# Performance work log

Measured on AMD Instinct MI355X. Metric: run time of the kernel, lower is better.

## Reference

```python
import jax, jax.numpy as jnp
import numpy as np

BN_EPS = 1e-5
K, D = 512, 64  # vocab_size, embed_dim


def conv2d(x, w, b, stride):
    y = jax.lax.conv_general_dilated(
        x, w, window_strides=(stride, stride), padding=[(1, 1), (1, 1)],
        dimension_numbers=("NCHW", "OIHW", "NCHW"))
    return y + b[None, :, None, None]


def batchnorm(x, g, b):
    # training-mode BN: batch statistics over (N, H, W)
    m = jnp.mean(x, axis=(0, 2, 3), keepdims=True)
    v = jnp.var(x, axis=(0, 2, 3), keepdims=True)
    return (x - m) * jax.lax.rsqrt(v + BN_EPS) * g[None, :, None, None] + b[None, :, None, None]


def setup_inputs() -> dict:
    key = jax.random.key(0)
    ks = jax.random.split(key, 8)
    dims = [3, 64, 128, 256]
    inp = {"x": jax.random.normal(ks[0], (32, 3, 256, 256), dtype=jnp.float32)}
    for i in range(3):
        cin, cout = dims[i], dims[i + 1]
        inp[f"w{i+1}"] = jax.random.normal(ks[i + 1], (cout, cin, 4, 4), dtype=jnp.float32) * 0.05
        inp[f"b{i+1}"] = jnp.zeros((cout,), dtype=jnp.float32)
        inp[f"g{i+1}"] = jnp.ones((cout,), dtype=jnp.float32)
        inp[f"be{i+1}"] = jnp.zeros((cout,), dtype=jnp.float32)
    inp["wq"] = jax.random.normal(ks[4], (D, 256, 1, 1), dtype=jnp.float32) * 0.05
    inp["bq"] = jnp.zeros((D,), dtype=jnp.float32)
    inp["codebook"] = jax.random.uniform(ks[5], (K, D), dtype=jnp.float32,
                                         minval=-1.0 / K, maxval=1.0 / K)
    return inp


def reference(x, w1, b1, g1, be1, w2, b2, g2, be2, w3, b3, g3, be3, wq, bq, codebook):
    commitment_cost = 0.25
    h = jax.nn.relu(batchnorm(conv2d(x, w1, b1, 2), g1, be1))
    h = jax.nn.relu(batchnorm(conv2d(h, w2, b2, 2), g2, be2))
    h = jax.nn.relu(batchnorm(conv2d(h, w3, b3, 2), g3, be3))
    z = conv2d(h, wq, bq, 1)                      # (B, D, H', W')

    zt = jnp.transpose(z, (0, 2, 3, 1))           # (B, H', W', D)
    z_flat = zt.reshape(-1, D)                    # (N, D)
    # squared L2 distances via expansion
    dists = (jnp.sum(z_flat ** 2, axis=1, keepdims=True)
             + jnp.sum(codebook ** 2, axis=1)
             - 2.0 * z_flat @ codebook.T)         # (N, K)
    idx = jnp.argmin(dists, axis=1)               # (N,)
    quantized = codebook[idx].reshape(zt.shape)   # gather == one-hot matmul

    e_latent = jnp.mean((jax.lax.stop_gradient(quantized) - zt) ** 2)
    q_latent = jnp.mean((quantized - jax.lax.stop_gradient(zt)) ** 2)
    loss = q_latent + commitment_cost * e_latent

    # straight-through estimator
    quantized = zt + jax.lax.stop_gradient(quantized - zt)

    counts = jnp.zeros((K,), dtype=jnp.float32).at[idx].add(1.0)
    avg_probs = counts / z_flat.shape[0]
    perplexity = jnp.exp(-jnp.sum(avg_probs * jnp.log(avg_probs + 1e-10)))

    symbols = jnp.transpose(quantized, (0, 3, 1, 2))  # (B, D, H', W')
    return symbols, loss, perplexity
```

## Files before the change

kernel.cpp:

```cpp
#include <hip/hip_runtime.h>
#include <hip/hip_bf16.h>


#define BATCH 32

#define SYM_N 2367488
#define NPX   36992.0
#define CHW   73984
#define HW2   1156

static const unsigned long long NEED1 = 201392128ull;
static const unsigned long long NEED2 = 100728832ull;

typedef _Float16 half4 __attribute__((ext_vector_type(4)));
typedef _Float16 half8 __attribute__((ext_vector_type(8)));
typedef float f32x16 __attribute__((ext_vector_type(16)));

__device__ __forceinline__ float ldv(const float* p) { return *p; }
__device__ __forceinline__ float ldv(const __hip_bfloat16* p) { return __bfloat162float(*p); }
__device__ __forceinline__ float ldv(const _Float16* p) { return (float)(*p); }
__device__ __forceinline__ void stv(float* p, float v) { *p = v; }
__device__ __forceinline__ void stv(__hip_bfloat16* p, float v) { *p = __float2bfloat16(v); }
__device__ __forceinline__ void stv(_Float16* p, float v) { *p = (_Float16)v; }

__device__ __forceinline__ void st4(float* p, float a, float b, float c, float d) {
    float4 v; v.x = a; v.y = b; v.z = c; v.w = d;
    *(float4*)p = v;
}
__device__ __forceinline__ void st4(_Float16* p, float a, float b, float c, float d) {
    union { _Float16 h[4]; ushort4 u; } t;
    t.h[0] = (_Float16)a; t.h[1] = (_Float16)b; t.h[2] = (_Float16)c; t.h[3] = (_Float16)d;
    *(ushort4*)p = t.u;
}

__global__ void initStatsK(double* statd, int* counts) {
    int i = threadIdx.x + blockIdx.x * blockDim.x;
    if (i < 1537) statd[i] = 0.0;
    if (i < 512) counts[i] = 0;
}

__global__ void csqK(const float* __restrict__ cb, float* __restrict__ csqf,
                     double* __restrict__ csqd) {
    int k = threadIdx.x + blockIdx.x * blockDim.x;
    if (k < 512) {
        const float* r = cb + (size_t)k * 64;
        float s = 0.f; double sd = 0.0;
        for (int d = 0; d < 64; ++d) {
            s = fmaf(r[d], r[d], s);
            sd += (double)r[d] * (double)r[d];
        }
        csqf[k] = s; csqd[k] = sd;
    }
}

__global__ void borderK(const double* __restrict__ csqd, int* __restrict__ kborder,
                        int* __restrict__ counts, double* __restrict__ lossAcc) {
    __shared__ double sV[512];
    __shared__ int sI[512];
    const int t = threadIdx.x;
    sV[t] = csqd[t]; sI[t] = t;
    __syncthreads();
    for (int st = 256; st > 0; st >>= 1) {
        if (t < st) {
            double v2 = sV[t + st]; int i2 = sI[t + st];
            if (v2 < sV[t] || (v2 == sV[t] && i2 < sI[t])) { sV[t] = v2; sI[t] = i2; }
        }
        __syncthreads();
    }
    if (t == 0) {
        int k = sI[0];
        *kborder = k;
        atomicAdd(&counts[k], 4224);
        atomicAdd(lossAcc, 4224.0 * sV[0]);
    }
}

__global__ __launch_bounds__(256) void fillK(const int* __restrict__ kborder,
                                             const float* __restrict__ cb,
                                             float* __restrict__ out) {
    const int kb = *kborder;
    int E = blockIdx.x * 256 + threadIdx.x;
    if (E < SYM_N) {
        int d = (E / HW2) & 63;
        out[E] = cb[(size_t)kb * 64 + d];
    }
}

template<int CIN, int COUT, int IH, int IW, bool BN_IN, bool STORE, bool STATS,
         typename TI, typename TO>
__global__ __launch_bounds__(256) void conv4x4s2K(
    const TI* __restrict__ in, const float* __restrict__ wgt,
    const float* __restrict__ bias,
    const float* __restrict__ inScale, const float* __restrict__ inShift,
    TO* __restrict__ out, double* __restrict__ gSum, double* __restrict__ gSq)
{
    constexpr int OH = IH / 2, OW = IW / 2;
    constexpr int COLB = OW / 16;
    __shared__ float sIn[8 * 18 * 34];
    __shared__ float sW[128 * 64];
    __shared__ float sStat[128];

    const int tid = threadIdx.x;
    const int tx = tid & 15, ty = tid >> 4;
    const int cog = ty & 7, rg = ty >> 3;
    const int n = blockIdx.z;
    const int coBase = blockIdx.y * 64;
    const int brow = blockIdx.x / COLB, bcol = blockIdx.x % COLB;
    const int oh0 = brow * 8, ow0 = bcol * 16;
    const int ihb = oh0 * 2 - 1, iwb = ow0 * 2 - 1;

    float acc[8][4];
#pragma unroll
    for (int j = 0; j < 8; ++j)
#pragma unroll
        for (int r = 0; r < 4; ++r) acc[j][r] = 0.f;

    for (int c0 = 0; c0 < CIN; c0 += 8) {
        const int CC = (CIN - c0 < 8) ? (CIN - c0) : 8;
        for (int i = tid; i < 8 * 18 * 34; i += 256) {
            int ci = i / 612; int rem = i - ci * 612;
            int ih = rem / 34; int iw = rem - ih * 34;
            float v = 0.f;
            int gh = ihb + ih, gw = iwb + iw;
            if (ci < CC && (unsigned)gh < (unsigned)IH && (unsigned)gw < (unsigned)IW) {
                float r0 = ldv(&in[(((size_t)n * CIN + (c0 + ci)) * IH + gh) * IW + gw]);
                if (BN_IN) r0 = fmaxf(fmaf(r0, inScale[c0 + ci], inShift[c0 + ci]), 0.f);
                v = r0;
            }
            sIn[i] = v;
        }
        for (int i = tid; i < 8192; i += 256) {
            int co = i >> 7, r = i & 127;
            int ci = r >> 4, t = r & 15;
            float v = 0.f;
            if (ci < CC) v = wgt[(((size_t)(coBase + co)) * CIN + (c0 + ci)) * 16 + t];
            sW[r * 64 + (co ^ ((r & 7) << 3))] = v;
        }
        __syncthreads();
        for (int ci = 0; ci < CC; ++ci) {
#pragma unroll
            for (int kh = 0; kh < 4; ++kh) {
#pragma unroll
                for (int kw = 0; kw < 4; ++kw) {
                    const int tap = kh * 4 + kw;
                    const float* wp = sW + (ci * 16 + tap) * 64 + ((cog * 8) ^ ((tap & 7) << 3));
                    float4 wa = *(const float4*)wp;
                    float4 wb = *(const float4*)(wp + 4);
                    const float* ip = sIn + (ci * 18 + rg * 8 + kh) * 34 + tx * 2 + kw;
                    float wv[8] = {wa.x, wa.y, wa.z, wa.w, wb.x, wb.y, wb.z, wb.w};
                    float iv[4] = {ip[0], ip[68], ip[136], ip[204]};
#pragma unroll
                    for (int j = 0; j < 8; ++j)
#pragma unroll
                        for (int r = 0; r < 4; ++r)
                            acc[j][r] = fmaf(wv[j], iv[r], acc[j][r]);
                }
            }
        }
        __syncthreads();
    }

    if (STATS) {
        if (tid < 128) sStat[tid] = 0.f;
        __syncthreads();
    }

    const int coG = coBase + cog * 8;
#pragma unroll
    for (int j = 0; j < 8; ++j) {
        float bv = bias[coG + j];
        float s = 0.f, s2 = 0.f;
#pragma unroll
        for (int r = 0; r < 4; ++r) {
            float v = acc[j][r] + bv;
            if (STORE)
                stv(&out[(((size_t)n * COUT + coG + j) * OH + (oh0 + rg * 4 + r)) * OW + ow0 + tx], v);
            s += v; s2 = fmaf(v, v, s2);
        }
        if (STATS) {
#pragma unroll
            for (int m = 1; m < 16; m <<= 1) {
                s  += __shfl_xor(s, m, 64);
                s2 += __shfl_xor(s2, m, 64);
            }
            if (tx == 0) {
                atomicAdd(&sStat[cog * 8 + j], s);
                atomicAdd(&sStat[64 + cog * 8 + j], s2);
            }
        }
    }
    if (STATS) {
        __syncthreads();
        if (tid < 64) {
            atomicAdd(&gSum[coBase + tid], (double)sStat[tid]);
            atomicAdd(&gSq[coBase + tid],  (double)sStat[64 + tid]);
        }
    }
}

template<int CIN, int COUT, int IH, int IW, int TH, int TW, bool BN_IN,
         bool STORE, bool STATS, typename TI, typename TO>
__global__ __launch_bounds__(256, 3) void conv8K(
    const TI* __restrict__ in, const float* __restrict__ wgt,
    const float* __restrict__ bias,
    const float* __restrict__ inScale, const float* __restrict__ inShift,
    TO* __restrict__ out, double* __restrict__ gSum, double* __restrict__ gSq)
{
    constexpr int OH = IH / 2, OW = IW / 2;
    constexpr int COLB = OW / TW;
    constexpr int SW = TW / 2;
    constexpr int ITH = TH * 2 + 2;
    constexpr int ITWP = TW * 2 + 4;
    constexpr int INSZ = 4 * ITH * ITWP;

    __shared__ float sIn[INSZ];
    __shared__ float sW[4 * 16 * 64];
    __shared__ float sStat[128];

    const int tid = threadIdx.x;
    const int s = tid & 31, cog = tid >> 5;
    const int sw = s & (SW - 1), sh = s / SW;
    const int n = blockIdx.z;
    const int coBase = blockIdx.y * 64;
    const int brow = blockIdx.x / COLB, bcol = blockIdx.x % COLB;
    const int oh0 = brow * TH, ow0 = bcol * TW;
    const int ihb = oh0 * 2 - 1, iwb = ow0 * 2 - 1;

    float acc[8][8];
#pragma unroll
    for (int c = 0; c < 8; ++c)
#pragma unroll
        for (int p = 0; p < 8; ++p) acc[c][p] = 0.f;

    for (int c0 = 0; c0 < CIN; c0 += 4) {
        const int CC = (CIN - c0 < 4) ? (CIN - c0) : 4;
        for (int i = tid; i < INSZ; i += 256) {
            int ci = i / (ITH * ITWP); int rem = i - ci * (ITH * ITWP);
            int ih = rem / ITWP; int iw = rem - ih * ITWP;
            float v = 0.f;
            int gh = ihb + ih, gw = iwb + iw;
            if (ci < CC && (unsigned)gh < (unsigned)IH && (unsigned)gw < (unsigned)IW) {
                float r0 = ldv(&in[(((size_t)n * CIN + (c0 + ci)) * IH + gh) * IW + gw]);
                if (BN_IN) r0 = fmaxf(fmaf(r0, inScale[c0 + ci], inShift[c0 + ci]), 0.f);
                v = r0;
            }
            sIn[i] = v;
        }
        for (int i = tid; i < 4096; i += 256) {
            int r = i >> 6, co = i & 63;
            int ci = r >> 4, tap = r & 15;
            float v = (ci < CC) ? wgt[(((size_t)(coBase + co)) * CIN + (c0 + ci)) * 16 + tap] : 0.f;
            sW[r * 64 + co] = v;
        }
        __syncthreads();
        for (int ci = 0; ci < CC; ++ci) {
#pragma unroll
            for (int kh = 0; kh < 4; ++kh) {
                float inv[4][8];
#pragma unroll
                for (int r = 0; r < 4; ++r) {
                    const float* ip = sIn + (ci * ITH + (sh * 4 + r) * 2 + kh) * ITWP + sw * 4;
                    float4 a = *(const float4*)ip;
                    float4 b = *(const float4*)(ip + 4);
                    inv[r][0] = a.x; inv[r][1] = a.y; inv[r][2] = a.z; inv[r][3] = a.w;
                    inv[r][4] = b.x; inv[r][5] = b.y; inv[r][6] = b.z; inv[r][7] = b.w;
                }
#pragma unroll
                for (int kw = 0; kw < 4; ++kw) {
                    const float* wp = sW + (ci * 16 + kh * 4 + kw) * 64 + cog * 8;
                    float4 wa = *(const float4*)wp;
                    float4 wb = *(const float4*)(wp + 4);
                    float wv[8] = {wa.x, wa.y, wa.z, wa.w, wb.x, wb.y, wb.z, wb.w};
#pragma unroll
                    for (int c = 0; c < 8; ++c)
#pragma unroll
                        for (int r = 0; r < 4; ++r)
#pragma unroll
                            for (int j = 0; j < 2; ++j)
                                acc[c][r * 2 + j] =
                                    fmaf(wv[c], inv[r][2 * j + kw], acc[c][r * 2 + j]);
                }
            }
        }
        __syncthreads();
    }

    if (STATS) {
        if (tid < 128) sStat[tid] = 0.f;
        __syncthreads();
    }

    const int coG = coBase + cog * 8;
#pragma unroll
    for (int c = 0; c < 8; ++c) {
        float bv = bias[coG + c];
        float s1 = 0.f, s2 = 0.f;
#pragma unroll
        for (int p = 0; p < 8; ++p) {
            float v = acc[c][p] + bv;
            int oh = oh0 + sh * 4 + (p >> 1), ow = ow0 + sw * 2 + (p & 1);
            if (STORE)
                stv(&out[(((size_t)n * COUT + coG + c) * OH + oh) * OW + ow], v);
            s1 += v; s2 = fmaf(v, v, s2);
        }
        if (STATS) {
#pragma unroll
            for (int m = 1; m < 32; m <<= 1) {
                s1 += __shfl_xor(s1, m, 64);
                s2 += __shfl_xor(s2, m, 64);
            }
            if ((tid & 31) == 0) {
                atomicAdd(&sStat[cog * 8 + c], s1);
                atomicAdd(&sStat[64 + cog * 8 + c], s2);
            }
        }
    }
    if (STATS) {
        __syncthreads();
        if (tid < 64) {
            atomicAdd(&gSum[coBase + tid], (double)sStat[tid]);
            atomicAdd(&gSq[coBase + tid],  (double)sStat[64 + tid]);
        }
    }
}

__global__ void bnFinK(const double* __restrict__ gSum, const double* __restrict__ gSq,
                       const float* __restrict__ g, const float* __restrict__ be,
                       float* __restrict__ scale, float* __restrict__ shift,
                       int C, double cnt)
{
    int c = threadIdx.x;
    if (c < C) {
        double m = gSum[c] / cnt;
        double v = gSq[c] / cnt - m * m;
        double sc = (double)g[c] / sqrt(v + 1e-5);
        scale[c] = (float)sc;
        shift[c] = (float)((double)be[c] - m * sc);
    }
}

__global__ __launch_bounds__(256) void splitWK(
    const float* __restrict__ w, _Float16* __restrict__ wsOut, int CIN, int COUT)
{
    int CH = CIN >> 4;
    int total = 16 * CH * COUT * 16;
    for (int i = blockIdx.x * 256 + threadIdx.x; i < total; i += gridDim.x * 256) {
        int cil = i & 15; int r = i >> 4;
        int co = r % COUT; r /= COUT;
        int c = r % CH; int tap = r / CH;
        int ci = c * 16 + cil;
        wsOut[i] = (_Float16)w[((size_t)co * CIN + ci) * 16 + tap];
    }
}

__global__ __launch_bounds__(256) void splitWqfK(
    const float* __restrict__ wq, _Float16* __restrict__ wqf)
{
    int i = blockIdx.x * 256 + threadIdx.x;
    int cil = i & 15; int r = i >> 4;
    int d = r & 63; int c0 = r >> 6;
    wqf[i] = (_Float16)wq[(size_t)d * 256 + c0 * 16 + cil];
}

__global__ __launch_bounds__(256) void cbhK(
    const float* __restrict__ cb, _Float16* __restrict__ cbh)
{
    int i = blockIdx.x * 256 + threadIdx.x;
    cbh[i] = (_Float16)cb[i];
}

template<int CIN, int COUT, int IH, int NF, bool BN_IN, typename TO>
__global__ __launch_bounds__(512) void convMfmaK(
    const _Float16* __restrict__ in, const _Float16* __restrict__ wsplit,
    const float* __restrict__ bias,
    const float* __restrict__ inScale, const float* __restrict__ inShift,
    TO* __restrict__ out, double* __restrict__ gSum, double* __restrict__ gSq)
{
    constexpr int OH = IH / 2;
    constexpr int OWB = OH / 32;
    constexpr int CH = CIN / 16;
    constexpr int ROW = 20;
    constexpr int ITW = 72;
    __shared__ _Float16 sA[10 * ITW * ROW];
    __shared__ float sStat[2 * COUT];

    const int tid = threadIdx.x;
    const int l = tid & 63, wid = tid >> 6;
    const int lane31 = l & 31, hs = l >> 5;
    const int mw = wid & 3, nw = wid >> 2;
    const int n = blockIdx.z;
    const int ohB = (blockIdx.x / OWB) * 4;
    const int owB = (blockIdx.x % OWB) * 32;
    const int ghBase = 2 * ohB - 1, gwA = 2 * owB - 4;

    for (int i = tid; i < 2 * COUT; i += 512) sStat[i] = 0.f;

    f32x16 acc[NF];
#pragma unroll
    for (int f = 0; f < NF; ++f)
#pragma unroll
        for (int j = 0; j < 16; ++j) acc[f][j] = 0.f;

    for (int c = 0; c < CH; ++c) {
        __syncthreads();
        for (int i = tid; i < 10 * 18 * 16; i += 512) {
            int iwq = i % 18; int r = i / 18; int ih = r % 10; int cil = r / 10;
            int gh = ghBase + ih;
            int gw0 = gwA + iwq * 4;
            float scv = 1.f, shv = 0.f;
            if (BN_IN) { scv = inScale[c * 16 + cil]; shv = inShift[c * 16 + cil]; }
            float vs[4] = {0.f, 0.f, 0.f, 0.f};
            if ((unsigned)gh < (unsigned)IH) {
                const _Float16* src = &in[(((size_t)n * CIN + c * 16 + cil) * IH + gh) * IH + gw0];
                if (gw0 >= 0 && gw0 + 3 < IH) {
                    half4 q4 = *(const half4*)src;
#pragma unroll
                    for (int e = 0; e < 4; ++e) {
                        float v = (float)q4[e];
                        if (BN_IN) v = fmaxf(fmaf(v, scv, shv), 0.f);
                        vs[e] = v;
                    }
                } else {
#pragma unroll
                    for (int e = 0; e < 4; ++e) {
                        int gw = gw0 + e;
                        if ((unsigned)gw < (unsigned)IH) {
                            float v = (float)src[e];
                            if (BN_IN) v = fmaxf(fmaf(v, scv, shv), 0.f);
                            vs[e] = v;
                        }
                    }
                }
            }
            _Float16* dst = &sA[(ih * ITW + iwq * 4) * ROW + cil];
            dst[0]       = (_Float16)vs[0];
            dst[ROW]     = (_Float16)vs[1];
            dst[2 * ROW] = (_Float16)vs[2];
            dst[3 * ROW] = (_Float16)vs[3];
        }
        __syncthreads();
#pragma unroll
        for (int kh = 0; kh < 4; ++kh) {
#pragma unroll
            for (int kw = 0; kw < 4; ++kw) {
                const int ihX = 2 * mw + kh;
                const int off = (ihX * ITW + 2 * lane31 + kw + 3) * ROW + hs * 8;
                half4 a0 = *(const half4*)&sA[off];
                half4 a1 = *(const half4*)&sA[off + 4];
                half8 a;
                a[0] = a0[0]; a[1] = a0[1]; a[2] = a0[2]; a[3] = a0[3];
                a[4] = a1[0]; a[5] = a1[1]; a[6] = a1[2]; a[7] = a1[3];
                const _Float16* bp = wsplit
                    + (((size_t)(kh * 4 + kw) * CH + c) * COUT + nw * (NF * 32) + lane31) * 16
                    + hs * 8;
#pragma unroll
                for (int f = 0; f < NF; ++f) {
                    half8 b = *(const half8*)(bp + (size_t)f * 32 * 16);
                    acc[f] = __builtin_amdgcn_mfma_f32_32x32x16_f16(a, b, acc[f], 0, 0, 0);
                }
            }
        }
    }

    const int oh = ohB + mw;
#pragma unroll
    for (int f = 0; f < NF; ++f) {
        int co = nw * (NF * 32) + f * 32 + lane31;
        float bv = bias[co];
        float s1 = 0.f, s2 = 0.f;
#pragma unroll
        for (int q = 0; q < 4; ++q) {
            float v0 = acc[f][q * 4 + 0] + bv;
            float v1 = acc[f][q * 4 + 1] + bv;
            float v2 = acc[f][q * 4 + 2] + bv;
            float v3 = acc[f][q * 4 + 3] + bv;
            s1 += (v0 + v1) + (v2 + v3);
            s2 = fmaf(v0, v0, s2); s2 = fmaf(v1, v1, s2);
            s2 = fmaf(v2, v2, s2); s2 = fmaf(v3, v3, s2);
            int ow = owB + q * 8 + hs * 4;
            st4(&out[(((size_t)n * COUT + co) * OH + oh) * OH + ow], v0, v1, v2, v3);
        }
        s1 += __shfl_xor(s1, 32, 64);
        s2 += __shfl_xor(s2, 32, 64);
        if (hs == 0) {
            atomicAdd(&sStat[co], s1);
            atomicAdd(&sStat[COUT + co], s2);
        }
    }
    __syncthreads();
    for (int i = tid; i < COUT; i += 512) {
        atomicAdd(&gSum[i], (double)sStat[i]);
        atomicAdd(&gSq[i],  (double)sStat[COUT + i]);
    }
}

template<int CIN, int COUT, int IH, int OWBn, int NF, bool BN_IN, typename TO>
__global__ __launch_bounds__(256) void convM1RK(
    const _Float16* __restrict__ in, const _Float16* __restrict__ wsplit,
    const float* __restrict__ bias,
    const float* __restrict__ inScale, const float* __restrict__ inShift,
    TO* __restrict__ out, double* __restrict__ gSum, double* __restrict__ gSq)
{
    constexpr int OH = IH / 2;
    constexpr int CH = CIN / 16;
    constexpr int ROW = 20;
    constexpr int ITW = 72;
    __shared__ _Float16 sA[4 * ITW * ROW];
    __shared__ float sStat[2 * COUT];

    const int tid = threadIdx.x;
    const int l = tid & 63, nw = tid >> 6;
    const int lane31 = l & 31, hs = l >> 5;
    const int n = blockIdx.z;
    const int oh = blockIdx.x / OWBn;
    const int owB = (blockIdx.x % OWBn) * 32;
    const int ghBase = 2 * oh - 1, gwA = 2 * owB - 4;

    for (int i = tid; i < 2 * COUT; i += 256) sStat[i] = 0.f;

    f32x16 acc[NF];
#pragma unroll
    for (int f = 0; f < NF; ++f)
#pragma unroll
        for (int j = 0; j < 16; ++j) acc[f][j] = 0.f;

    for (int c = 0; c < CH; ++c) {
        __syncthreads();
        for (int i = tid; i < 4 * 18 * 16; i += 256) {
            int iwq = i % 18; int r = i / 18; int ih = r & 3; int cil = r >> 2;
            int gh = ghBase + ih;
            int gw0 = gwA + iwq * 4;
            float scv = 1.f, shv = 0.f;
            if (BN_IN) { scv = inScale[c * 16 + cil]; shv = inShift[c * 16 + cil]; }
            float vs[4] = {0.f, 0.f, 0.f, 0.f};
            if ((unsigned)gh < (unsigned)IH) {
                const _Float16* src = &in[(((size_t)n * CIN + c * 16 + cil) * IH + gh) * IH + gw0];
                if (gw0 >= 0 && gw0 + 3 < IH) {
                    half4 q4 = *(const half4*)src;
#pragma unroll
                    for (int e = 0; e < 4; ++e) {
                        float v = (float)q4[e];
                        if (BN_IN) v = fmaxf(fmaf(v, scv, shv), 0.f);
                        vs[e] = v;
                    }
                } else {
#pragma unroll
                    for (int e = 0; e < 4; ++e) {
                        int gw = gw0 + e;
                        if ((unsigned)gw < (unsigned)IH) {
                            float v = (float)src[e];
                            if (BN_IN) v = fmaxf(fmaf(v, scv, shv), 0.f);
                            vs[e] = v;
                        }
                    }
                }
            }
            _Float16* dst = &sA[(ih * ITW + iwq * 4) * ROW + cil];
            dst[0]       = (_Float16)vs[0];
            dst[ROW]     = (_Float16)vs[1];
            dst[2 * ROW] = (_Float16)vs[2];
            dst[3 * ROW] = (_Float16)vs[3];
        }
        __syncthreads();
#pragma unroll
        for (int kh = 0; kh < 4; ++kh) {
#pragma unroll
            for (int kw = 0; kw < 4; ++kw) {
                const int off = (kh * ITW + 2 * lane31 + kw + 3) * ROW + hs * 8;
                half4 a0 = *(const half4*)&sA[off];
                half4 a1 = *(const half4*)&sA[off + 4];
                half8 a;
                a[0] = a0[0]; a[1] = a0[1]; a[2] = a0[2]; a[3] = a0[3];
                a[4] = a1[0]; a[5] = a1[1]; a[6] = a1[2]; a[7] = a1[3];
                const _Float16* bp = wsplit
                    + (((size_t)(kh * 4 + kw) * CH + c) * COUT + nw * (NF * 32) + lane31) * 16
                    + hs * 8;
#pragma unroll
                for (int f = 0; f < NF; ++f) {
                    half8 b = *(const half8*)(bp + (size_t)f * 32 * 16);
                    acc[f] = __builtin_amdgcn_mfma_f32_32x32x16_f16(a, b, acc[f], 0, 0, 0);
                }
            }
        }
    }

#pragma unroll
    for (int f = 0; f < NF; ++f) {
        int co = nw * (NF * 32) + f * 32 + lane31;
        float bv = bias[co];
        float s1 = 0.f, s2 = 0.f;
#pragma unroll
        for (int q = 0; q < 4; ++q) {
            float v0 = acc[f][q * 4 + 0] + bv;
            float v1 = acc[f][q * 4 + 1] + bv;
            float v2 = acc[f][q * 4 + 2] + bv;
            float v3 = acc[f][q * 4 + 3] + bv;
            s1 += (v0 + v1) + (v2 + v3);
            s2 = fmaf(v0, v0, s2); s2 = fmaf(v1, v1, s2);
            s2 = fmaf(v2, v2, s2); s2 = fmaf(v3, v3, s2);
            int ow = owB + q * 8 + hs * 4;
            st4(&out[(((size_t)n * COUT + co) * OH + oh) * OH + ow], v0, v1, v2, v3);
        }
        s1 += __shfl_xor(s1, 32, 64);
        s2 += __shfl_xor(s2, 32, 64);
        if (hs == 0) {
            atomicAdd(&sStat[co], s1);
            atomicAdd(&sStat[COUT + co], s2);
        }
    }
    __syncthreads();
    for (int i = tid; i < COUT; i += 256) {
        atomicAdd(&gSum[i], (double)sStat[i]);
        atomicAdd(&gSq[i],  (double)sStat[COUT + i]);
    }
}

__global__ __launch_bounds__(512) void headK4(
    const _Float16* __restrict__ y3h, const _Float16* __restrict__ wqf,
    const float* __restrict__ bq,
    const float* __restrict__ sc3, const float* __restrict__ sh3,
    const float* __restrict__ cb, const _Float16* __restrict__ cbh,
    const float* __restrict__ csqf,
    float* __restrict__ out, int* __restrict__ counts,
    double* __restrict__ lossAcc)
{
    __shared__ _Float16 sH[32 * 264];
    __shared__ float    sZ[32 * 68];
    __shared__ _Float16 sZh[32 * 72];
    __shared__ float    sCS[8 * 32];
    __shared__ int      sCI[8 * 32];

    const int tid = threadIdx.x;
    const int w = tid >> 6;
    const int l = tid & 63;
    const int lane31 = l & 31, hs = l >> 5;
    const int blk = blockIdx.x;
    const int n = (blk * 32) >> 10;
    const int hw0 = (blk * 32) & 1023;

    {
        const int px = tid & 31, cg = tid >> 5;
#pragma unroll
        for (int k = 0; k < 16; ++k) {
            int c = cg + 16 * k;
            float v = (float)y3h[(((size_t)n * 256 + c) << 10) + hw0 + px];
            v = fmaxf(fmaf(v, sc3[c], sh3[c]), 0.f);
            sH[px * 264 + c] = (_Float16)v;
        }
    }
    __syncthreads();

    if (w < 2) {
        f32x16 za;
#pragma unroll
        for (int j = 0; j < 16; ++j) za[j] = 0.f;
#pragma unroll
        for (int c0 = 0; c0 < 16; ++c0) {
            half8 a = *(const half8*)&sH[lane31 * 264 + c0 * 16 + hs * 8];
            const _Float16* bp = wqf + ((size_t)(c0 * 64) + 32 * w + lane31) * 16 + hs * 8;
            half8 b = *(const half8*)bp;
            za = __builtin_amdgcn_mfma_f32_32x32x16_f16(a, b, za, 0, 0, 0);
        }
        const int d = 32 * w + lane31;
        const float bqv = bq[d];
#pragma unroll
        for (int j = 0; j < 16; ++j) {
            int row = (j & 3) + 8 * (j >> 2) + 4 * hs;
            float zv = za[j] + bqv;
            sZ[row * 68 + d] = zv;
            sZh[row * 72 + d] = (_Float16)zv;
        }
    }
    __syncthreads();

    f32x16 acc0, acc1;
#pragma unroll
    for (int j = 0; j < 16; ++j) { acc0[j] = 0.f; acc1[j] = 0.f; }
#pragma unroll
    for (int ks = 0; ks < 4; ++ks) {
        half8 a = *(const half8*)&sZh[lane31 * 72 + ks * 16 + hs * 8];
        const _Float16* b0 = cbh + ((size_t)(64 * w + lane31) << 6) + ks * 16 + hs * 8;
        const _Float16* b1 = b0 + (32 << 6);
        acc0 = __builtin_amdgcn_mfma_f32_32x32x16_f16(a, *(const half8*)b0, acc0, 0, 0, 0);
        acc1 = __builtin_amdgcn_mfma_f32_32x32x16_f16(a, *(const half8*)b1, acc1, 0, 0, 0);
    }
    const int cw0 = 64 * w + lane31;
    const float cs0 = csqf[cw0], cs1 = csqf[cw0 + 32];
#pragma unroll
    for (int j = 0; j < 16; ++j) {
        int row = (j & 3) + 8 * (j >> 2) + 4 * hs;
        float s = cs0 - 2.f * acc0[j];
        int idx = cw0;
        float s1 = cs1 - 2.f * acc1[j];
        if (s1 < s) { s = s1; idx = cw0 + 32; }
#pragma unroll
        for (int m = 1; m < 32; m <<= 1) {
            float so = __shfl_xor(s, m, 32);
            int io = __shfl_xor(idx, m, 32);
            if (so < s || (so == s && io < idx)) { s = so; idx = io; }
        }
        if (lane31 == 0) { sCS[w * 32 + row] = s; sCI[w * 32 + row] = idx; }
    }
    __syncthreads();

    if (w == 0 && l < 32) {
        const int px = l;
        float best = sCS[px]; int bidx = sCI[px];
#pragma unroll
        for (int g = 1; g < 8; ++g) {
            float b = sCS[g * 32 + px]; int i = sCI[g * 32 + px];
            if (b < best || (b == best && i < bidx)) { best = b; bidx = i; }
        }
        atomicAdd(&counts[bidx], 1);

        const int hw = hw0 + px;
        const int hh = hw >> 5, ww = hw & 31;
        const int obase = n * CHW + (hh + 1) * 34 + (ww + 1);
        const float4* qp = (const float4*)(cb + ((size_t)bidx << 6));
        const float4* zrow = (const float4*)(sZ + px * 68);
        float sq = 0.f;
#pragma unroll
        for (int q = 0; q < 16; ++q) {
            float4 c4 = qp[q];
            float4 z4 = zrow[q];
            float d0 = c4.x - z4.x, d1 = c4.y - z4.y;
            float d2 = c4.z - z4.z, d3 = c4.w - z4.w;
            sq = fmaf(d0, d0, sq); sq = fmaf(d1, d1, sq);
            sq = fmaf(d2, d2, sq); sq = fmaf(d3, d3, sq);
            out[obase + (4 * q + 0) * HW2] = c4.x;
            out[obase + (4 * q + 1) * HW2] = c4.y;
            out[obase + (4 * q + 2) * HW2] = c4.z;
            out[obase + (4 * q + 3) * HW2] = c4.w;
        }
#pragma unroll
        for (int m = 1; m < 32; m <<= 1) sq += __shfl_xor(sq, m, 32);
        if (l == 0) atomicAdd(lossAcc, (double)sq);
    }
}

__global__ __launch_bounds__(128) void convqK(
    const float* __restrict__ y3, const float* __restrict__ wq,
    const float* __restrict__ bq,
    const float* __restrict__ sc3, const float* __restrict__ sh3,
    float* __restrict__ z)
{
    __shared__ float sWq[64 * 68];
    __shared__ float sS[64], sH[64];
    const int tid = threadIdx.x;
    const int px = blockIdx.x * 128 + tid;
    const int n = px >> 10, hw = px & 1023;

    float accv[64];
#pragma unroll
    for (int d = 0; d < 64; ++d) accv[d] = 0.f;

    const float* base = y3 + (((size_t)n * 256) << 10) + hw;
    for (int c0 = 0; c0 < 256; c0 += 64) {
        __syncthreads();
        for (int i = tid; i < 4096; i += 128) {
            int c = i & 63, d = i >> 6;
            sWq[c * 68 + d] = wq[(size_t)d * 256 + c0 + c];
        }
        if (tid < 64) { sS[tid] = sc3[c0 + tid]; sH[tid] = sh3[c0 + tid]; }
        __syncthreads();
        for (int c = 0; c < 64; ++c) {
            float h = base[(size_t)(c0 + c) << 10];
            h = fmaxf(fmaf(h, sS[c], sH[c]), 0.f);
            const float4* wrow = (const float4*)(sWq + c * 68);
#pragma unroll
            for (int q = 0; q < 16; ++q) {
                float4 w4 = wrow[q];
                accv[4*q+0] = fmaf(h, w4.x, accv[4*q+0]);
                accv[4*q+1] = fmaf(h, w4.y, accv[4*q+1]);
                accv[4*q+2] = fmaf(h, w4.z, accv[4*q+2]);
                accv[4*q+3] = fmaf(h, w4.w, accv[4*q+3]);
            }
        }
    }
    float* zo = z + (size_t)px * 64;
    const float4* bq4 = (const float4*)bq;
#pragma unroll
    for (int q = 0; q < 16; ++q) {
        float4 b4 = bq4[q];
        float4 v;
        v.x = accv[4*q+0] + b4.x; v.y = accv[4*q+1] + b4.y;
        v.z = accv[4*q+2] + b4.z; v.w = accv[4*q+3] + b4.w;
        ((float4*)zo)[q] = v;
    }
}

__global__ __launch_bounds__(256) void vqK(
    const float* __restrict__ z, const float* __restrict__ cb,
    const float* __restrict__ csqf, float* __restrict__ out,
    int* __restrict__ counts, double* __restrict__ lossAcc)
{
    const int tid = threadIdx.x;
    const int lane = tid & 63;
    const int grp = tid >> 6;
    const int px = blockIdx.x * 64 + lane;

    float zr[64];
    const float4* zp = (const float4*)(z + (size_t)px * 64);
#pragma unroll
    for (int q = 0; q < 16; ++q) {
        float4 t = zp[q];
        zr[4*q] = t.x; zr[4*q+1] = t.y; zr[4*q+2] = t.z; zr[4*q+3] = t.w;
    }

    const int kbase = grp * 128;
    float best = 3.4e38f; int bidx = kbase;
    for (int kk = 0; kk < 128; ++kk) {
        const float4* crow = (const float4*)(cb + (size_t)(kbase + kk) * 64);
        float d0 = 0.f, d1 = 0.f, d2 = 0.f, d3 = 0.f;
#pragma unroll
        for (int q = 0; q < 16; ++q) {
            float4 c4 = crow[q];
            d0 = fmaf(zr[4*q+0], c4.x, d0);
            d1 = fmaf(zr[4*q+1], c4.y, d1);
            d2 = fmaf(zr[4*q+2], c4.z, d2);
            d3 = fmaf(zr[4*q+3], c4.w, d3);
        }
        float dot = (d0 + d1) + (d2 + d3);
        float score = csqf[kbase + kk] - 2.0f * dot;
        if (score < best) { best = score; bidx = kbase + kk; }
    }

    __shared__ float sB[256];
    __shared__ int   sI[256];
    sB[tid] = best; sI[tid] = bidx;
    __syncthreads();
    if (grp == 0) {
#pragma unroll
        for (int g = 1; g < 4; ++g) {
            float b = sB[lane + 64 * g]; int i = sI[lane + 64 * g];
            if (b < best || (b == best && i < bidx)) { best = b; bidx = i; }
        }
        atomicAdd(&counts[bidx], 1);

        const int n = px >> 10, hw = px & 1023;
        const int h = hw >> 5, w = hw & 31;
        const int obase = n * CHW + (h + 1) * 34 + (w + 1);
        const float4* qp = (const float4*)(cb + (size_t)bidx * 64);
        float sq = 0.f;
#pragma unroll
        for (int q = 0; q < 16; ++q) {
            float4 c4 = qp[q];
            float vv[4] = {c4.x, c4.y, c4.z, c4.w};
#pragma unroll
            for (int j = 0; j < 4; ++j) {
                int d = 4 * q + j;
                float df = vv[j] - zr[d];
                sq = fmaf(df, df, sq);
                out[obase + d * HW2] = vv[j];
            }
        }
#pragma unroll
        for (int m = 1; m < 64; m <<= 1) sq += __shfl_xor(sq, m, 64);
        if (lane == 0) atomicAdd(lossAcc, (double)sq);
    }
}

__global__ void finalizeK(const int* __restrict__ counts,
                          const double* __restrict__ lossAcc,
                          float* __restrict__ out)
{
    const int tid = threadIdx.x;
    double ent = 0.0;
    for (int k = tid; k < 512; k += 64) {
        double p = (double)counts[k] / NPX;
        ent -= p * log(p + 1e-10);
    }
#pragma unroll
    for (int m = 1; m < 64; m <<= 1) ent += __shfl_xor(ent, m, 64);
    if (tid == 0) {
        out[SYM_N]     = (float)(1.25 * lossAcc[0] / (double)SYM_N);
        out[SYM_N + 1] = (float)exp(ent);
    }
}

__global__ __launch_bounds__(256) void zeroOutK(float* __restrict__ out, int n) {
    int i = blockIdx.x * 256 + threadIdx.x;
    if (i < n) out[i] = 0.0f;
}
__global__ void sentinelK(float* out, float lossv, float perpv) {
    if (threadIdx.x == 0) { out[SYM_N] = lossv; out[SYM_N + 1] = perpv; }
}

static void run_mfma(void* const* d_in, float* out, char* ws, hipStream_t stream)
{
    const float* x   = (const float*)d_in[0];
    const float* w1  = (const float*)d_in[1];
    const float* b1  = (const float*)d_in[2];
    const float* g1  = (const float*)d_in[3];
    const float* be1 = (const float*)d_in[4];
    const float* w2  = (const float*)d_in[5];
    const float* b2  = (const float*)d_in[6];
    const float* g2  = (const float*)d_in[7];
    const float* be2 = (const float*)d_in[8];
    const float* w3  = (const float*)d_in[9];
    const float* b3  = (const float*)d_in[10];
    const float* g3  = (const float*)d_in[11];
    const float* be3 = (const float*)d_in[12];
    const float* wq  = (const float*)d_in[13];
    const float* bq  = (const float*)d_in[14];
    const float* cb  = (const float*)d_in[15];

    double* statd  = (double*)(ws);
    float*  sscale = (float*)(ws + 16384);
    int*    counts = (int*)(ws + 24576);
    float*  csqf   = (float*)(ws + 28672);
    double* csqd   = (double*)(ws + 30720);
    int*    kbord  = (int*)(ws + 34816);
    double* lossAcc = statd + 1536;

    char* A0 = ws + 65536;
    _Float16* y1h = (_Float16*)A0;
    _Float16* y2h = (_Float16*)(A0 + 67108864ull);
    _Float16* y3h = (_Float16*)(A0 + 100663296ull);
    _Float16* w2s = (_Float16*)(A0 + 117440512ull);
    _Float16* w3s = (_Float16*)(A0 + 117702656ull);
    _Float16* wqf = (_Float16*)(A0 + 118751232ull);
    _Float16* cbh = (_Float16*)(A0 + 118800384ull);

    initStatsK<<<7, 256, 0, stream>>>(statd, counts);
    csqK<<<2, 256, 0, stream>>>(cb, csqf, csqd);
    borderK<<<1, 512, 0, stream>>>(csqd, kbord, counts, lossAcc);
    fillK<<<(SYM_N + 255) / 256, 256, 0, stream>>>(kbord, cb, out);
    splitWK<<<512, 256, 0, stream>>>(w2, w2s, 64, 128);
    splitWK<<<2048, 256, 0, stream>>>(w3, w3s, 128, 256);
    splitWqfK<<<64, 256, 0, stream>>>(wq, wqf);
    cbhK<<<128, 256, 0, stream>>>(cb, cbh);

    conv8K<3, 64, 256, 256, 8, 32, false, true, true, float, _Float16>
        <<<dim3(64, 1, BATCH), 256, 0, stream>>>(
        x, w1, b1, nullptr, nullptr, y1h, statd + 0, statd + 256);
    bnFinK<<<1, 256, 0, stream>>>(statd + 0, statd + 256, g1, be1,
                                  sscale + 0, sscale + 256, 64, 524288.0);

    convMfmaK<64, 128, 128, 2, true, _Float16>
        <<<dim3(32, 1, BATCH), 512, 0, stream>>>(
        y1h, w2s, b2, sscale + 0, sscale + 256, y2h, statd + 512, statd + 768);
    bnFinK<<<1, 256, 0, stream>>>(statd + 512, statd + 768, g2, be2,
                                  sscale + 512, sscale + 768, 128, 131072.0);

    convM1RK<128, 256, 64, 1, 2, true, _Float16>
        <<<dim3(32, 1, BATCH), 256, 0, stream>>>(
        y2h, w3s, b3, sscale + 512, sscale + 768, y3h, statd + 1024, statd + 1280);
    bnFinK<<<1, 256, 0, stream>>>(statd + 1024, statd + 1280, g3, be3,
                                  sscale + 1024, sscale + 1280, 256, 32768.0);

    headK4<<<1024, 512, 0, stream>>>(y3h, wqf, bq, sscale + 1024, sscale + 1280,
                                     cb, cbh, csqf, out, counts, lossAcc);
    finalizeK<<<1, 64, 0, stream>>>(counts, lossAcc, out);
}

static void run_fast_bf16(void* const* d_in, float* out, char* ws, hipStream_t stream)
{
    const float* x   = (const float*)d_in[0];
    const float* w1  = (const float*)d_in[1];
    const float* b1  = (const float*)d_in[2];
    const float* g1  = (const float*)d_in[3];
    const float* be1 = (const float*)d_in[4];
    const float* w2  = (const float*)d_in[5];
    const float* b2  = (const float*)d_in[6];
    const float* g2  = (const float*)d_in[7];
    const float* be2 = (const float*)d_in[8];
    const float* w3  = (const float*)d_in[9];
    const float* b3  = (const float*)d_in[10];
    const float* g3  = (const float*)d_in[11];
    const float* be3 = (const float*)d_in[12];
    const float* wq  = (const float*)d_in[13];
    const float* bq  = (const float*)d_in[14];
    const float* cb  = (const float*)d_in[15];

    double* statd  = (double*)(ws);
    float*  sscale = (float*)(ws + 16384);
    int*    counts = (int*)(ws + 24576);
    float*  csqf   = (float*)(ws + 28672);
    double* csqd   = (double*)(ws + 30720);
    int*    kbord  = (int*)(ws + 34816);
    double* lossAcc = statd + 1536;

    __hip_bfloat16* y1 = (__hip_bfloat16*)(ws + 65536);
    __hip_bfloat16* y2 = (__hip_bfloat16*)(ws + 65536 + 67108864ull);
    float* y3 = (float*)(ws + 65536);
    float* z  = (float*)(ws + 65536 + 33554432ull);

    initStatsK<<<7, 256, 0, stream>>>(statd, counts);
    csqK<<<2, 256, 0, stream>>>(cb, csqf, csqd);
    borderK<<<1, 512, 0, stream>>>(csqd, kbord, counts, lossAcc);
    fillK<<<(SYM_N + 255) / 256, 256, 0, stream>>>(kbord, cb, out);

    conv4x4s2K<3, 64, 256, 256, false, true, true, float, __hip_bfloat16>
        <<<dim3(128, 1, BATCH), 256, 0, stream>>>(
        x, w1, b1, nullptr, nullptr, y1, statd + 0, statd + 256);
    bnFinK<<<1, 256, 0, stream>>>(statd + 0, statd + 256, g1, be1,
                                  sscale + 0, sscale + 256, 64, 524288.0);

    conv8K<64, 128, 128, 128, 8, 32, true, true, true, __hip_bfloat16, __hip_bfloat16>
        <<<dim3(16, 2, BATCH), 256, 0, stream>>>(
        y1, w2, b2, sscale + 0, sscale + 256, y2, statd + 512, statd + 768);
    bnFinK<<<1, 256, 0, stream>>>(statd + 512, statd + 768, g2, be2,
                                  sscale + 512, sscale + 768, 128, 131072.0);

    conv8K<128, 256, 64, 64, 16, 16, true, true, true, __hip_bfloat16, float>
        <<<dim3(4, 4, BATCH), 256, 0, stream>>>(
        y2, w3, b3, sscale + 512, sscale + 768, y3, statd + 1024, statd + 1280);
    bnFinK<<<1, 256, 0, stream>>>(statd + 1024, statd + 1280, g3, be3,
                                  sscale + 1024, sscale + 1280, 256, 32768.0);

    convqK<<<256, 128, 0, stream>>>(y3, wq, bq, sscale + 1024, sscale + 1280, z);
    vqK<<<512, 256, 0, stream>>>(z, cb, csqf, out, counts, lossAcc);
    finalizeK<<<1, 64, 0, stream>>>(counts, lossAcc, out);
}

extern "C" void kernel_launch(void* const* d_in, const int* in_sizes, int n_in,
                              void* d_out, int out_size, void* d_ws, size_t ws_size,
                              hipStream_t stream)
{
    float* out = (float*)d_out;
    char* ws = (char*)d_ws;

    if (ws_size >= NEED1) {
        run_mfma(d_in, out, ws, stream);
    } else if (ws_size >= NEED2) {
        run_fast_bf16(d_in, out, ws, stream);
    } else {
        zeroOutK<<<(SYM_N + 2 + 255) / 256, 256, 0, stream>>>(out, SYM_N + 2);
        sentinelK<<<1, 64, 0, stream>>>(out, -4444.0f, -5555.0f);
    }
}
```

Before: 338.3 us.

## Replace scalar first conv with MFMA-based fp16 conv kernel

Replaces the scalar conv8K first-layer convolution with a new conv1MK kernel. It stages an fp16 input tile in shared memory and computes each input channel's 4x4 taps as one 32x32x16 MFMA. A small pre-kernel reorders w1 into fp16 tap-major layout. The aim is to move the largest-spatial convolution onto matrix cores. In exchange the input and weights are rounded to fp16, and the launch uses more, smaller blocks with atomic BN-stat accumulation.

```diff
diff --git a/kernel.cpp b/kernel.cpp
--- a/kernel.cpp
+++ b/kernel.cpp
@@ -353,6 +353,17 @@
     }
 }
 
+__global__ __launch_bounds__(256) void splitW1fK(
+    const float* __restrict__ w1, _Float16* __restrict__ w1f)
+{
+    int i = blockIdx.x * 256 + threadIdx.x;
+    if (i < 3072) {
+        int tap = i & 15; int r = i >> 4;
+        int co = r & 63; int ci = r >> 6;
+        w1f[i] = (_Float16)w1[((size_t)co * 3 + ci) * 16 + tap];
+    }
+}
+
 __global__ __launch_bounds__(256) void splitWqfK(
     const float* __restrict__ wq, _Float16* __restrict__ wqf)
 {
@@ -367,6 +378,105 @@
 {
     int i = blockIdx.x * 256 + threadIdx.x;
     cbh[i] = (_Float16)cb[i];
+}
+
+__global__ __launch_bounds__(256) void conv1MK(
+    const float* __restrict__ x, const _Float16* __restrict__ w1f,
+    const float* __restrict__ bias,
+    _Float16* __restrict__ out, double* __restrict__ gSum, double* __restrict__ gSq)
+{
+    constexpr int IH = 256, OH = 128, ITW = 72;
+    __shared__ _Float16 sA[3 * 10 * ITW];
+    __shared__ float sStat[128];
+
+    const int tid = threadIdx.x;
+    const int l = tid & 63, mw = tid >> 6;
+    const int lane31 = l & 31, hs = l >> 5;
+    const int n = blockIdx.z;
+    const int oh0 = (blockIdx.x >> 2) * 4;
+    const int owB = (blockIdx.x & 3) * 32;
+    const int ghBase = 2 * oh0 - 1, gwA = 2 * owB - 4;
+
+    if (tid < 128) sStat[tid] = 0.f;
+
+    for (int i = tid; i < 540; i += 256) {
+        int q = i % 18; int r = i / 18; int ih = r % 10; int ci = r / 10;
+        int gh = ghBase + ih;
+        int gw0 = gwA + q * 4;
+        float vs[4] = {0.f, 0.f, 0.f, 0.f};
+        if ((unsigned)gh < (unsigned)IH) {
+            const float* src = &x[(((size_t)n * 3 + ci) * IH + gh) * IH + gw0];
+            if (gw0 >= 0 && gw0 + 3 < IH) {
+                float4 f4 = *(const float4*)src;
+                vs[0] = f4.x; vs[1] = f4.y; vs[2] = f4.z; vs[3] = f4.w;
+            } else {
+#pragma unroll
+                for (int e = 0; e < 4; ++e) {
+                    int gw = gw0 + e;
+                    if ((unsigned)gw < (unsigned)IH) vs[e] = src[e];
+                }
+            }
+        }
+        union { _Float16 h[4]; ushort4 u; } t;
+        t.h[0] = (_Float16)vs[0]; t.h[1] = (_Float16)vs[1];
+        t.h[2] = (_Float16)vs[2]; t.h[3] = (_Float16)vs[3];
+        *(ushort4*)&sA[(ci * 10 + ih) * ITW + q * 4] = t.u;
+    }
+    __syncthreads();
+
+    f32x16 acc[2];
+#pragma unroll
+    for (int f = 0; f < 2; ++f)
+#pragma unroll
+        for (int j = 0; j < 16; ++j) acc[f][j] = 0.f;
+
+#pragma unroll
+    for (int ci = 0; ci < 3; ++ci) {
+        half8 a;
+#pragma unroll
+        for (int khp = 0; khp < 2; ++khp) {
+            const _Float16* row = &sA[(ci * 10 + 2 * mw + 2 * hs + khp) * ITW + 2 * lane31 + 3];
+#pragma unroll
+            for (int kw = 0; kw < 4; ++kw) a[khp * 4 + kw] = row[kw];
+        }
+        const _Float16* bp = w1f + ((size_t)ci * 64 + lane31) * 16 + hs * 8;
+#pragma unroll
+        for (int f = 0; f < 2; ++f) {
+            half8 b = *(const half8*)(bp + (size_t)f * 32 * 16);
+            acc[f] = __builtin_amdgcn_mfma_f32_32x32x16_f16(a, b, acc[f], 0, 0, 0);
+        }
+    }
+
+    const int oh = oh0 + mw;
+#pragma unroll
+    for (int f = 0; f < 2; ++f) {
+        int co = f * 32 + lane31;
+        float bv = bias[co];
+        float s1 = 0.f, s2 = 0.f;
+#pragma unroll
+        for (int q = 0; q < 4; ++q) {
+            float v0 = acc[f][q * 4 + 0] + bv;
+            float v1 = acc[f][q * 4 + 1] + bv;
+            float v2 = acc[f][q * 4 + 2] + bv;
+            float v3 = acc[f][q * 4 + 3] + bv;
+            s1 += (v0 + v1) + (v2 + v3);
+            s2 = fmaf(v0, v0, s2); s2 = fmaf(v1, v1, s2);
+            s2 = fmaf(v2, v2, s2); s2 = fmaf(v3, v3, s2);
+            int ow = owB + q * 8 + hs * 4;
+            st4(&out[(((size_t)n * 64 + co) * OH + oh) * OH + ow], v0, v1, v2, v3);
+        }
+        s1 += __shfl_xor(s1, 32, 64);
+        s2 += __shfl_xor(s2, 32, 64);
+        if (hs == 0) {
+            atomicAdd(&sStat[co], s1);
+            atomicAdd(&sStat[64 + co], s2);
+        }
+    }
+    __syncthreads();
+    if (tid < 64) {
+        atomicAdd(&gSum[tid], (double)sStat[tid]);
+        atomicAdd(&gSq[tid],  (double)sStat[64 + tid]);
+    }
 }
 
 template<int CIN, int COUT, int IH, int NF, bool BN_IN, typename TO>
@@ -921,6 +1031,7 @@
     _Float16* w3s = (_Float16*)(A0 + 117702656ull);
     _Float16* wqf = (_Float16*)(A0 + 118751232ull);
     _Float16* cbh = (_Float16*)(A0 + 118800384ull);
+    _Float16* w1f = (_Float16*)(A0 + 118865920ull);
 
     initStatsK<<<7, 256, 0, stream>>>(statd, counts);
     csqK<<<2, 256, 0, stream>>>(cb, csqf, csqd);
@@ -930,10 +1041,10 @@
     splitWK<<<2048, 256, 0, stream>>>(w3, w3s, 128, 256);
     splitWqfK<<<64, 256, 0, stream>>>(wq, wqf);
     cbhK<<<128, 256, 0, stream>>>(cb, cbh);
-
-    conv8K<3, 64, 256, 256, 8, 32, false, true, true, float, _Float16>
-        <<<dim3(64, 1, BATCH), 256, 0, stream>>>(
-        x, w1, b1, nullptr, nullptr, y1h, statd + 0, statd + 256);
+    splitW1fK<<<12, 256, 0, stream>>>(w1, w1f);
+
+    conv1MK<<<dim3(128, 1, BATCH), 256, 0, stream>>>(
+        x, w1f, b1, y1h, statd + 0, statd + 256);
     bnFinK<<<1, 256, 0, stream>>>(statd + 0, statd + 256, g1, be1,
                                   sscale + 0, sscale + 256, 64, 524288.0);
 
```

Measured after the change: 360.5 us. 1.07x slower.
